# Optimization experiments

Measured on AMD Instinct MI355X. Metric: run time of the kernel, lower is better.

Reference implementation:

```python
import jax, jax.numpy as jnp
import numpy as np
import math

D_MODEL = 1024
N_HEADS = 16
SEQ = 1024
BATCH = 4


def setup_inputs() -> dict:
    key = jax.random.key(0)
    ks = jax.random.split(key, 13)
    s = 1.0 / math.sqrt(D_MODEL)  # keep logits in a sane range
    return {
        "x": jax.random.normal(ks[0], (BATCH, SEQ, D_MODEL), jnp.float32),
        "Wq": jax.random.normal(ks[1], (D_MODEL, D_MODEL), jnp.float32) * s,
        "bq": jnp.zeros((D_MODEL,), jnp.float32),
        "Wk": jax.random.normal(ks[2], (D_MODEL, D_MODEL), jnp.float32) * s,
        "bk": jnp.zeros((D_MODEL,), jnp.float32),
        "Wv": jax.random.normal(ks[3], (D_MODEL, D_MODEL), jnp.float32) * s,
        "bv": jnp.zeros((D_MODEL,), jnp.float32),
        "Wo": jax.random.normal(ks[4], (D_MODEL, D_MODEL), jnp.float32) * s,
        "bo": jnp.zeros((D_MODEL,), jnp.float32),
        "Wimp": jax.random.normal(ks[5], (N_HEADS, D_MODEL), jnp.float32) * s,
        "bimp": jnp.zeros((N_HEADS,), jnp.float32),
        "k_ema": jax.random.normal(ks[6], (SEQ, D_MODEL), jnp.float32),
        "v_ema": jax.random.normal(ks[7], (SEQ, D_MODEL), jnp.float32),
    }


def reference(x, Wq, bq, Wk, bk, Wv, bv, Wo, bo, Wimp, bimp, k_ema, v_ema):
    B, S, D = x.shape
    H = Wimp.shape[0]
    hd = D // H

    def proj(W, b):
        # [B,S,D] -> [B,H,S,hd]
        return (x @ W.T + b).reshape(B, S, H, hd).transpose(0, 2, 1, 3)

    q = proj(Wq, bq)
    k = proj(Wk, bk)
    v = proj(Wv, bv)

    scores = jnp.einsum("bhqd,bhkd->bhqk", q, k) / math.sqrt(hd)

    # importance bias: outer-sum of per-head key/value importance vectors
    k_imp = (k_ema[:S] @ Wimp.T + bimp).T  # [H, S]
    v_imp = (v_ema[:S] @ Wimp.T + bimp).T  # [H, S]
    bias = 0.5 * (k_imp[:, :, None] + v_imp[:, None, :])  # [H, S, S]
    scores = scores + 0.1 * bias[None]

    # causal mask (torch masks before bias add; -inf + finite == -inf, so equivalent)
    causal = jnp.triu(jnp.ones((S, S), bool), k=1)
    scores = jnp.where(causal, -jnp.inf, scores)

    attn = jax.nn.softmax(scores, axis=-1)
    out = jnp.einsum("bhqk,bhkd->bhqd", attn, v)
    out = out.transpose(0, 2, 1, 3).reshape(B, S, D)
    return out @ Wo.T + bo
```

## Files before the change

### kernel.cpp

```cpp
#include <hip/hip_runtime.h>
#include <hip/hip_bf16.h>
#include <math.h>

#define D_MODEL 1024
#define SEQ     1024
#define BATCH   4
#define NHEADS  16
#define HD      64

#define QSC 0.18033688f
#define BSC 0.072134752f

typedef __bf16 bf16x8 __attribute__((ext_vector_type(8)));
typedef __bf16 bf16x4 __attribute__((ext_vector_type(4)));
typedef float  f32x4  __attribute__((ext_vector_type(4)));

__device__ __forceinline__ f32x4 mfma16(bf16x8 a, bf16x8 b, f32x4 c) {
  return __builtin_amdgcn_mfma_f32_16x16x32_bf16(a, b, c, 0, 0, 0);
}

__device__ __forceinline__ void async16(__bf16* lds, const __bf16* g) {
  __builtin_amdgcn_global_load_lds(g, lds, 16, 0, 0);
}

__global__ __launch_bounds__(256) void prep_kernel(
    const float* __restrict__ x,
    const float* __restrict__ Wq, const float* __restrict__ Wk,
    const float* __restrict__ Wv, const float* __restrict__ Wo,
    const float* __restrict__ v_ema,
    const float* __restrict__ Wimp, const float* __restrict__ bimp,
    __bf16* __restrict__ x_bf, __bf16* __restrict__ wq_bf, __bf16* __restrict__ wk_bf,
    __bf16* __restrict__ wv_bf, __bf16* __restrict__ wo_bf,
    float* __restrict__ vimp) {
  const int bid = blockIdx.x;
  const int tid = threadIdx.x;
  if (bid < 4096) {
    int i = bid * 256 + tid;
    float4 v = ((const float4*)x)[i];
    bf16x4 o; o[0] = (__bf16)v.x; o[1] = (__bf16)v.y; o[2] = (__bf16)v.z; o[3] = (__bf16)v.w;
    ((bf16x4*)x_bf)[i] = o;
  } else if (bid < 8192) {
    int i = (bid - 4096) * 256 + tid;
    int sel = i >> 18;
    int j = i & 262143;
    const float* s = (sel == 0) ? Wq : (sel == 1) ? Wk : (sel == 2) ? Wv : Wo;
    __bf16* d      = (sel == 0) ? wq_bf : (sel == 1) ? wk_bf : (sel == 2) ? wv_bf : wo_bf;
    float4 v = ((const float4*)s)[j];
    bf16x4 o; o[0] = (__bf16)v.x; o[1] = (__bf16)v.y; o[2] = (__bf16)v.z; o[3] = (__bf16)v.w;
    ((bf16x4*)d)[j] = o;
  } else {
    const int s    = (bid - 8192) * 4 + (tid >> 6);
    const int lane = tid & 63;
    const float4* ve = (const float4*)(v_ema + (size_t)s * D_MODEL);
    float acc0 = 0.f, acc1 = 0.f, acc2 = 0.f, acc3 = 0.f;
    float acc4 = 0.f, acc5 = 0.f, acc6 = 0.f, acc7 = 0.f;
    float acc8 = 0.f, acc9 = 0.f, accA = 0.f, accB = 0.f;
    float accC = 0.f, accD = 0.f, accE = 0.f, accF = 0.f;
    #pragma unroll
    for (int i = 0; i < 4; i++) {
      const int c = lane + i * 64;
      float4 v = ve[c];
      #define VIMP_H(H, ACC)                                                     \
        {                                                                        \
          float4 w = ((const float4*)(Wimp + (H) * D_MODEL))[c];                 \
          ACC += v.x * w.x + v.y * w.y + v.z * w.z + v.w * w.w;                  \
        }
      VIMP_H(0, acc0)  VIMP_H(1, acc1)  VIMP_H(2, acc2)  VIMP_H(3, acc3)
      VIMP_H(4, acc4)  VIMP_H(5, acc5)  VIMP_H(6, acc6)  VIMP_H(7, acc7)
      VIMP_H(8, acc8)  VIMP_H(9, acc9)  VIMP_H(10, accA) VIMP_H(11, accB)
      VIMP_H(12, accC) VIMP_H(13, accD) VIMP_H(14, accE) VIMP_H(15, accF)
      #undef VIMP_H
    }
    #define VIMP_RED(ACC)                                                        \
      for (int mm = 32; mm >= 1; mm >>= 1) ACC += __shfl_xor(ACC, mm);
    VIMP_RED(acc0) VIMP_RED(acc1) VIMP_RED(acc2) VIMP_RED(acc3)
    VIMP_RED(acc4) VIMP_RED(acc5) VIMP_RED(acc6) VIMP_RED(acc7)
    VIMP_RED(acc8) VIMP_RED(acc9) VIMP_RED(accA) VIMP_RED(accB)
    VIMP_RED(accC) VIMP_RED(accD) VIMP_RED(accE) VIMP_RED(accF)
    #undef VIMP_RED
    if (lane == 0) {
      vimp[0  * SEQ + s] = acc0 + bimp[0];  vimp[1  * SEQ + s] = acc1 + bimp[1];
      vimp[2  * SEQ + s] = acc2 + bimp[2];  vimp[3  * SEQ + s] = acc3 + bimp[3];
      vimp[4  * SEQ + s] = acc4 + bimp[4];  vimp[5  * SEQ + s] = acc5 + bimp[5];
      vimp[6  * SEQ + s] = acc6 + bimp[6];  vimp[7  * SEQ + s] = acc7 + bimp[7];
      vimp[8  * SEQ + s] = acc8 + bimp[8];  vimp[9  * SEQ + s] = acc9 + bimp[9];
      vimp[10 * SEQ + s] = accA + bimp[10]; vimp[11 * SEQ + s] = accB + bimp[11];
      vimp[12 * SEQ + s] = accC + bimp[12]; vimp[13 * SEQ + s] = accD + bimp[13];
      vimp[14 * SEQ + s] = accE + bimp[14]; vimp[15 * SEQ + s] = accF + bimp[15];
    }
  }
}

template<bool OUT_BF16>
__global__ __launch_bounds__(256) void gemm_bt(
    const __bf16* __restrict__ A,
    const __bf16* __restrict__ W0, const __bf16* __restrict__ W1, const __bf16* __restrict__ W2,
    const float* __restrict__ b0, const float* __restrict__ b1, const float* __restrict__ b2,
    void* out0, void* out1, void* out2, float sc0, float sc1, float sc2) {
  const int z = blockIdx.z;
  const __bf16* W   = (z == 0) ? W0 : (z == 1) ? W1 : W2;
  const float* bias = (z == 0) ? b0 : (z == 1) ? b1 : b2;
  void* out         = (z == 0) ? out0 : (z == 1) ? out1 : out2;
  const float sc    = (z == 0) ? sc0 : (z == 1) ? sc1 : sc2;

  __shared__ __bf16 As[4 * 4096];
  __shared__ __bf16 Bs[4 * 4096];

  const int tid = threadIdx.x;
  const int w = tid >> 6, l = tid & 63;
  const int quad = l >> 4, l16 = l & 15;
  const int wy = w >> 1, wx = w & 1;
  const int row0 = blockIdx.y * 128;
  const int col0 = blockIdx.x * 128;

  const f32x4 fzero = {0.f, 0.f, 0.f, 0.f};
  f32x4 acc[4][4];
  for (int i = 0; i < 4; i++)
    for (int j = 0; j < 4; j++) acc[i][j] = fzero;

  const int lr = l >> 2;
  const int sw0 = (((l & 3) ^ (lr & 3)) * 8);
  const int rowA = w * 16 + lr;
  const __bf16* aptr = A + (size_t)(row0 + rowA) * D_MODEL + sw0;
  const __bf16* bptr = W + (size_t)(col0 + rowA) * D_MODEL + sw0;
  const int ldsOff = w * 512 + l * 8;

  const int rswz = (quad ^ (l16 & 3)) * 8;

  #pragma unroll
  for (int p = 0; p < 3; ++p) {
    const int off = p << 12;
    const int kk = p * 32;
    async16(&As[off + ldsOff], aptr + kk);
    async16(&As[off + 2048 + ldsOff], aptr + (size_t)64 * D_MODEL + kk);
    async16(&Bs[off + ldsOff], bptr + kk);
    async16(&Bs[off + 2048 + ldsOff], bptr + (size_t)64 * D_MODEL + kk);
  }

  #pragma unroll 4
  for (int t = 0; t < 32; ++t) {
    const int rb = (t & 3) << 12;
    if (t < 29) {
      const int sb = ((t + 3) & 3) << 12;
      const int kk = (t + 3) * 32;
      async16(&As[sb + ldsOff], aptr + kk);
      async16(&As[sb + 2048 + ldsOff], aptr + (size_t)64 * D_MODEL + kk);
      async16(&Bs[sb + ldsOff], bptr + kk);
      async16(&Bs[sb + 2048 + ldsOff], bptr + (size_t)64 * D_MODEL + kk);
      asm volatile("s_waitcnt vmcnt(12)" ::: "memory");
    } else if (t == 29) {
      asm volatile("s_waitcnt vmcnt(8)" ::: "memory");
    } else if (t == 30) {
      asm volatile("s_waitcnt vmcnt(4)" ::: "memory");
    } else {
      asm volatile("s_waitcnt vmcnt(0)" ::: "memory");
    }
    __builtin_amdgcn_s_barrier();
    bf16x8 af[4], bfr[4];
    #pragma unroll
    for (int mi = 0; mi < 4; mi++) af[mi]  = *(const bf16x8*)&As[rb + (wy * 64 + mi * 16 + l16) * 32 + rswz];
    #pragma unroll
    for (int ni = 0; ni < 4; ni++) bfr[ni] = *(const bf16x8*)&Bs[rb + (wx * 64 + ni * 16 + l16) * 32 + rswz];
    if (z == 1) {
      #pragma unroll
      for (int mi = 0; mi < 4; mi++)
        #pragma unroll
        for (int ni = 0; ni < 4; ni++)
          acc[mi][ni] = mfma16(bfr[ni], af[mi], acc[mi][ni]);
    } else {
      #pragma unroll
      for (int mi = 0; mi < 4; mi++)
        #pragma unroll
        for (int ni = 0; ni < 4; ni++)
          acc[mi][ni] = mfma16(af[mi], bfr[ni], acc[mi][ni]);
    }
    __builtin_amdgcn_s_barrier();
  }

  if (z == 1 && OUT_BF16) {
    __bf16* kp = (__bf16*)out;
    #pragma unroll
    for (int ni = 0; ni < 4; ni++) {
      const int wcolbase = col0 + wx * 64 + ni * 16 + quad * 4;
      const float4 b4 = *(const float4*)&bias[wcolbase];
      const float bb[4] = {b4.x, b4.y, b4.z, b4.w};
      #pragma unroll
      for (int mi = 0; mi < 4; mi++) {
        const int token = row0 + wy * 64 + mi * 16 + l16;
        const int bh = (token >> 10) * 16 + (wcolbase >> 6);
        const int colp = ((wcolbase & 63) + ((token & 7) << 3)) & 63;
        union { __bf16 hh[4]; uint2 uu; } pk;
        #pragma unroll
        for (int r = 0; r < 4; r++) pk.hh[r] = (__bf16)(acc[mi][ni][r] + bb[r]);
        *(uint2*)(kp + ((size_t)bh * SEQ + (token & 1023)) * HD + colp) = pk.uu;
      }
    }
  } else if (z == 2 && OUT_BF16) {
    __bf16* vp = (__bf16*)out;
    #pragma unroll
    for (int ni = 0; ni < 4; ni++) {
      const int col = col0 + wx * 64 + ni * 16 + l16;
      const float bv = bias[col];
      #pragma unroll
      for (int mi = 0; mi < 4; mi++) {
        const int token = row0 + wy * 64 + mi * 16 + quad * 4;
        const int bh = (token >> 10) * 16 + (col >> 6);
        const int chk = (token >> 6) & 15;
        const int keyp = ((token & 63) + ((col & 7) << 3)) & 63;
        const size_t base = (((size_t)bh * 16 + chk) * 64 + (col & 63)) * 64 + keyp;
        union { __bf16 hh[4]; uint2 uu; } pk;
        #pragma unroll
        for (int r = 0; r < 4; r++) pk.hh[r] = (__bf16)(acc[mi][ni][r] + bv);
        *(uint2*)(vp + base) = pk.uu;
      }
    }
  } else {
    #pragma unroll
    for (int ni = 0; ni < 4; ni++) {
      const int col = col0 + wx * 64 + ni * 16 + l16;
      const float bv = bias[col];
      #pragma unroll
      for (int mi = 0; mi < 4; mi++) {
        const int row = row0 + wy * 64 + mi * 16 + quad * 4;
        #pragma unroll
        for (int r = 0; r < 4; r++) {
          float v = (acc[mi][ni][r] + bv) * sc;
          if (OUT_BF16) ((__bf16*)out)[(size_t)(row + r) * D_MODEL + col] = (__bf16)v;
          else          ((float*)out)[(size_t)(row + r) * D_MODEL + col] = v;
        }
      }
    }
  }
}

__global__ __launch_bounds__(256, 2) void attn_kernel(
    const __bf16* __restrict__ Qb, const __bf16* __restrict__ Kp,
    const __bf16* __restrict__ Vp, const float* __restrict__ vimp,
    __bf16* __restrict__ Ob) {
  const int id = blockIdx.x;
  const int bh = id & 63;
  const int gg = id >> 6;
  const int b = bh >> 4, h = bh & 15;
  const int tid = threadIdx.x;
  const int wave = tid >> 6, lane = tid & 63;
  const int quad = lane >> 4, l16 = lane & 15;

  __shared__ __bf16 Kl[2][4096];
  __shared__ __bf16 Vl[2][4096];
  __shared__ __bf16 Ps[4][16][72];

  const __bf16* kbase = Kp + (size_t)bh * (SEQ * HD);
  const __bf16* vbase = Vp + (size_t)bh * (SEQ * HD);
  const float* vimpH = vimp + h * SEQ;

  const int rot0 = ((quad + (l16 & 7)) & 7) * 8;
  const int rot1 = ((quad + 4 + (l16 & 7)) & 7) * 8;
  const int frow = l16 * 64;

  #pragma unroll 1
  for (int grp = 0; grp < 2; grp++) {
    const int g = grp ? (15 - gg) : gg;
    const int nch = g + 1;
    const int qrow = g * 64 + wave * 16 + l16;
    const __bf16* qp = Qb + (size_t)(b * SEQ + qrow) * D_MODEL + h * HD;
    bf16x8 qa0 = *(const bf16x8*)(qp + quad * 8);
    bf16x8 qa1 = *(const bf16x8*)(qp + 32 + quad * 8);
    float l_i = 0.f;
    f32x4 o[4];
    #pragma unroll
    for (int td = 0; td < 4; td++) { o[td][0] = 0.f; o[td][1] = 0.f; o[td][2] = 0.f; o[td][3] = 0.f; }

    __syncthreads();
    async16(&Kl[0][tid * 8], kbase + tid * 8);
    async16(&Kl[0][2048 + tid * 8], kbase + 2048 + tid * 8);
    async16(&Vl[0][tid * 8], vbase + tid * 8);
    async16(&Vl[0][2048 + tid * 8], vbase + 2048 + tid * 8);

    for (int ch = 0; ch < nch; ch++) {
      const int buf = ch & 1;
      __syncthreads();
      if (ch + 1 < nch) {
        const __bf16* gk = kbase + (ch + 1) * 4096;
        const __bf16* gv = vbase + (ch + 1) * 4096;
        const int nb = buf ^ 1;
        async16(&Kl[nb][tid * 8], gk + tid * 8);
        async16(&Kl[nb][2048 + tid * 8], gk + 2048 + tid * 8);
        async16(&Vl[nb][tid * 8], gv + tid * 8);
        async16(&Vl[nb][2048 + tid * 8], gv + 2048 + tid * 8);
      }
      const int kc = ch * 64;
      float4 vi[4];
      #pragma unroll
      for (int t = 0; t < 4; t++) vi[t] = *(const float4*)(vimpH + kc + t * 16 + quad * 4);
      bf16x8 kf0[4], kf1[4];
      #pragma unroll
      for (int t = 0; t < 4; t++) {
        kf0[t] = *(const bf16x8*)&Kl[buf][t * 1024 + frow + rot0];
        kf1[t] = *(const bf16x8*)&Kl[buf][t * 1024 + frow + rot1];
      }
      bf16x8 vfr0[4], vfr1[4];
      #pragma unroll
      for (int td = 0; td < 4; td++) {
        vfr0[td] = *(const bf16x8*)&Vl[buf][td * 1024 + frow + rot0];
        vfr1[td] = *(const bf16x8*)&Vl[buf][td * 1024 + frow + rot1];
      }
      const f32x4 fz = {0.f, 0.f, 0.f, 0.f};
      float p[4][4];
      float lsum = 0.f;
      if (ch == nch - 1) {
        #pragma unroll
        for (int t = 0; t < 4; t++) {
          f32x4 sacc = fz;
          sacc = mfma16(kf0[t], qa0, sacc);
          sacc = mfma16(kf1[t], qa1, sacc);
          const float vib[4] = {vi[t].x, vi[t].y, vi[t].z, vi[t].w};
          #pragma unroll
          for (int r = 0; r < 4; r++) {
            float pp = exp2f(sacc[r] + BSC * vib[r]);
            pp = (kc + t * 16 + quad * 4 + r <= qrow) ? pp : 0.f;
            p[t][r] = pp;
            lsum += pp;
          }
        }
      } else {
        #pragma unroll
        for (int t = 0; t < 4; t++) {
          f32x4 sacc = fz;
          sacc = mfma16(kf0[t], qa0, sacc);
          sacc = mfma16(kf1[t], qa1, sacc);
          const float vib[4] = {vi[t].x, vi[t].y, vi[t].z, vi[t].w};
          #pragma unroll
          for (int r = 0; r < 4; r++) {
            float pp = exp2f(sacc[r] + BSC * vib[r]);
            p[t][r] = pp;
            lsum += pp;
          }
        }
      }
      l_i += lsum;
      #pragma unroll
      for (int t = 0; t < 4; t++) {
        union { __bf16 hh[4]; uint2 uu; } pk;
        #pragma unroll
        for (int r = 0; r < 4; r++) pk.hh[r] = (__bf16)p[t][r];
        *(uint2*)&Ps[wave][l16][t * 16 + quad * 4] = pk.uu;
      }
      bf16x8 pf0 = *(const bf16x8*)&Ps[wave][l16][quad * 8];
      bf16x8 pf1 = *(const bf16x8*)&Ps[wave][l16][32 + quad * 8];
      #pragma unroll
      for (int td = 0; td < 4; td++) {
        o[td] = mfma16(vfr0[td], pf0, o[td]);
        o[td] = mfma16(vfr1[td], pf1, o[td]);
      }
    }

    float L = l_i;
    L += __shfl_xor(L, 16);
    L += __shfl_xor(L, 32);
    const float il = 1.0f / L;
    __bf16* op = Ob + (size_t)(b * SEQ + qrow) * D_MODEL + h * HD;
    #pragma unroll
    for (int td = 0; td < 4; td++) {
      union { __bf16 hh[4]; uint2 uu; } pk;
      #pragma unroll
      for (int r = 0; r < 4; r++) pk.hh[r] = (__bf16)(o[td][r] * il);
      *(uint2*)(op + td * 16 + quad * 4) = pk.uu;
    }
  }
}

extern "C" void kernel_launch(void* const* d_in, const int* in_sizes, int n_in,
                              void* d_out, int out_size, void* d_ws, size_t ws_size,
                              hipStream_t stream) {
  const float* x     = (const float*)d_in[0];
  const float* Wq    = (const float*)d_in[1];
  const float* bq    = (const float*)d_in[2];
  const float* Wk    = (const float*)d_in[3];
  const float* bk    = (const float*)d_in[4];
  const float* Wv    = (const float*)d_in[5];
  const float* bv    = (const float*)d_in[6];
  const float* Wo    = (const float*)d_in[7];
  const float* bo    = (const float*)d_in[8];
  const float* Wimp  = (const float*)d_in[9];
  const float* bimp  = (const float*)d_in[10];
  const float* v_ema = (const float*)d_in[12];
  float* out = (float*)d_out;

  char* ws = (char*)d_ws;
  __bf16* x_bf  = (__bf16*)(ws);
  __bf16* wq_bf = (__bf16*)(ws + (8ull  << 20));
  __bf16* wk_bf = (__bf16*)(ws + (10ull << 20));
  __bf16* wv_bf = (__bf16*)(ws + (12ull << 20));
  __bf16* wo_bf = (__bf16*)(ws + (14ull << 20));
  __bf16* q_bf  = (__bf16*)(ws + (16ull << 20));
  __bf16* kp_bf = (__bf16*)(ws + (24ull << 20));
  __bf16* vp_bf = (__bf16*)(ws + (32ull << 20));
  __bf16* a_bf  = (__bf16*)(ws + (40ull << 20));
  float*  vimp  = (float*)(ws + (48ull << 20));

  prep_kernel<<<8448, 256, 0, stream>>>(
      x, Wq, Wk, Wv, Wo, v_ema, Wimp, bimp,
      x_bf, wq_bf, wk_bf, wv_bf, wo_bf, vimp);

  gemm_bt<true><<<dim3(8, 32, 3), 256, 0, stream>>>(
      x_bf, wq_bf, wk_bf, wv_bf, bq, bk, bv,
      (void*)q_bf, (void*)kp_bf, (void*)vp_bf, QSC, 1.0f, 1.0f);

  attn_kernel<<<dim3(512), 256, 0, stream>>>(
      q_bf, kp_bf, vp_bf, vimp, a_bf);

  gemm_bt<false><<<dim3(8, 32, 1), 256, 0, stream>>>(
      a_bf, wo_bf, wo_bf, wo_bf, bo, bo, bo,
      (void*)out, (void*)out, (void*)out, 1.0f, 1.0f, 1.0f);
}
```

Before: 208.7 us.

## Triple-buffer K/V pipeline across both causal query groups and vectorize GEMM epilogue stores

The attention kernel now runs the two query groups as one continuous 17-chunk stream. It uses a three-slot LDS ring for K/V tiles with prefetch distance 2 and explicit vmcnt waits in place of the per-chunk __syncthreads. The vimp bias loads are prefetched one chunk ahead, and the output is flushed when the first group finishes. The GEMM epilogue swaps MFMA operand order for the Q/output paths so each lane holds 4 consecutive columns, allowing vector bias loads and 8-byte or 16-byte stores in place of scalar strided stores. The cost is more LDS per block, which may affect occupancy, plus more complex indexing.

Result: no change. 212.8 us (+2.0%).

```diff
diff --git a/kernel.cpp b/kernel.cpp
--- a/kernel.cpp
+++ b/kernel.cpp
@@ -161,7 +161,7 @@
     for (int mi = 0; mi < 4; mi++) af[mi]  = *(const bf16x8*)&As[rb + (wy * 64 + mi * 16 + l16) * 32 + rswz];
     #pragma unroll
     for (int ni = 0; ni < 4; ni++) bfr[ni] = *(const bf16x8*)&Bs[rb + (wx * 64 + ni * 16 + l16) * 32 + rswz];
-    if (z == 1) {
+    if (z != 2) {
       #pragma unroll
       for (int mi = 0; mi < 4; mi++)
         #pragma unroll
@@ -214,20 +214,37 @@
         *(uint2*)(vp + base) = pk.uu;
       }
     }
+  } else if (OUT_BF16) {
+    __bf16* qo = (__bf16*)out;
+    #pragma unroll
+    for (int ni = 0; ni < 4; ni++) {
+      const int wcb = col0 + wx * 64 + ni * 16 + quad * 4;
+      const float4 b4 = *(const float4*)&bias[wcb];
+      const float bb[4] = {b4.x, b4.y, b4.z, b4.w};
+      #pragma unroll
+      for (int mi = 0; mi < 4; mi++) {
+        const int token = row0 + wy * 64 + mi * 16 + l16;
+        union { __bf16 hh[4]; uint2 uu; } pk;
+        #pragma unroll
+        for (int r = 0; r < 4; r++) pk.hh[r] = (__bf16)((acc[mi][ni][r] + bb[r]) * sc);
+        *(uint2*)(qo + (size_t)token * D_MODEL + wcb) = pk.uu;
+      }
+    }
   } else {
+    float* fo = (float*)out;
     #pragma unroll
     for (int ni = 0; ni < 4; ni++) {
-      const int col = col0 + wx * 64 + ni * 16 + l16;
-      const float bv = bias[col];
+      const int wcb = col0 + wx * 64 + ni * 16 + quad * 4;
+      const float4 b4 = *(const float4*)&bias[wcb];
       #pragma unroll
       for (int mi = 0; mi < 4; mi++) {
-        const int row = row0 + wy * 64 + mi * 16 + quad * 4;
-        #pragma unroll
-        for (int r = 0; r < 4; r++) {
-          float v = (acc[mi][ni][r] + bv) * sc;
-          if (OUT_BF16) ((__bf16*)out)[(size_t)(row + r) * D_MODEL + col] = (__bf16)v;
-          else          ((float*)out)[(size_t)(row + r) * D_MODEL + col] = v;
-        }
+        const int token = row0 + wy * 64 + mi * 16 + l16;
+        float4 vv;
+        vv.x = (acc[mi][ni][0] + b4.x) * sc;
+        vv.y = (acc[mi][ni][1] + b4.y) * sc;
+        vv.z = (acc[mi][ni][2] + b4.z) * sc;
+        vv.w = (acc[mi][ni][3] + b4.w) * sc;
+        *(float4*)(fo + (size_t)token * D_MODEL + wcb) = vv;
       }
     }
   }
@@ -245,8 +262,8 @@
   const int wave = tid >> 6, lane = tid & 63;
   const int quad = lane >> 4, l16 = lane & 15;
 
-  __shared__ __bf16 Kl[2][4096];
-  __shared__ __bf16 Vl[2][4096];
+  __shared__ __bf16 Kl[3][4096];
+  __shared__ __bf16 Vl[3][4096];
   __shared__ __bf16 Ps[4][16][72];
 
   const __bf16* kbase = Kp + (size_t)bh * (SEQ * HD);
@@ -257,115 +274,164 @@
   const int rot1 = ((quad + 4 + (l16 & 7)) & 7) * 8;
   const int frow = l16 * 64;
 
+  const int g0 = gg, g1 = 15 - gg;
+  const int n0 = g0 + 1;
+
+  const int qrow0 = g0 * 64 + wave * 16 + l16;
+  const int qrow1 = g1 * 64 + wave * 16 + l16;
+  const __bf16* qp0 = Qb + (size_t)(b * SEQ + qrow0) * D_MODEL + h * HD;
+  const __bf16* qp1 = Qb + (size_t)(b * SEQ + qrow1) * D_MODEL + h * HD;
+  bf16x8 qA0 = *(const bf16x8*)(qp0 + quad * 8);
+  bf16x8 qA1 = *(const bf16x8*)(qp0 + 32 + quad * 8);
+  bf16x8 qB0 = *(const bf16x8*)(qp1 + quad * 8);
+  bf16x8 qB1 = *(const bf16x8*)(qp1 + 32 + quad * 8);
+
+  async16(&Kl[0][tid * 8], kbase + tid * 8);
+  async16(&Kl[0][2048 + tid * 8], kbase + 2048 + tid * 8);
+  async16(&Vl[0][tid * 8], vbase + tid * 8);
+  async16(&Vl[0][2048 + tid * 8], vbase + 2048 + tid * 8);
+  float4 vi_c[4];
+  #pragma unroll
+  for (int t = 0; t < 4; t++) vi_c[t] = *(const float4*)(vimpH + t * 16 + quad * 4);
+  __builtin_amdgcn_sched_barrier(0);
+  {
+    const int ck1 = (1 <= g0) ? 1 : 0;
+    const __bf16* gk = kbase + (size_t)ck1 * 4096;
+    const __bf16* gv = vbase + (size_t)ck1 * 4096;
+    async16(&Kl[1][tid * 8], gk + tid * 8);
+    async16(&Kl[1][2048 + tid * 8], gk + 2048 + tid * 8);
+    async16(&Vl[1][tid * 8], gv + tid * 8);
+    async16(&Vl[1][2048 + tid * 8], gv + 2048 + tid * 8);
+  }
+
+  float l_i = 0.f;
+  f32x4 o[4];
+  #pragma unroll
+  for (int td = 0; td < 4; td++) { o[td][0] = 0.f; o[td][1] = 0.f; o[td][2] = 0.f; o[td][3] = 0.f; }
+  int qrow = qrow0;
+  bf16x8 cqa0 = qA0, cqa1 = qA1;
+
   #pragma unroll 1
-  for (int grp = 0; grp < 2; grp++) {
-    const int g = grp ? (15 - gg) : gg;
-    const int nch = g + 1;
-    const int qrow = g * 64 + wave * 16 + l16;
-    const __bf16* qp = Qb + (size_t)(b * SEQ + qrow) * D_MODEL + h * HD;
-    bf16x8 qa0 = *(const bf16x8*)(qp + quad * 8);
-    bf16x8 qa1 = *(const bf16x8*)(qp + 32 + quad * 8);
-    float l_i = 0.f;
-    f32x4 o[4];
-    #pragma unroll
-    for (int td = 0; td < 4; td++) { o[td][0] = 0.f; o[td][1] = 0.f; o[td][2] = 0.f; o[td][3] = 0.f; }
-
-    __syncthreads();
-    async16(&Kl[0][tid * 8], kbase + tid * 8);
-    async16(&Kl[0][2048 + tid * 8], kbase + 2048 + tid * 8);
-    async16(&Vl[0][tid * 8], vbase + tid * 8);
-    async16(&Vl[0][2048 + tid * 8], vbase + 2048 + tid * 8);
-
-    for (int ch = 0; ch < nch; ch++) {
-      const int buf = ch & 1;
-      __syncthreads();
-      if (ch + 1 < nch) {
-        const __bf16* gk = kbase + (ch + 1) * 4096;
-        const __bf16* gv = vbase + (ch + 1) * 4096;
-        const int nb = buf ^ 1;
-        async16(&Kl[nb][tid * 8], gk + tid * 8);
-        async16(&Kl[nb][2048 + tid * 8], gk + 2048 + tid * 8);
-        async16(&Vl[nb][tid * 8], gv + tid * 8);
-        async16(&Vl[nb][2048 + tid * 8], gv + 2048 + tid * 8);
-      }
-      const int kc = ch * 64;
-      float4 vi[4];
-      #pragma unroll
-      for (int t = 0; t < 4; t++) vi[t] = *(const float4*)(vimpH + kc + t * 16 + quad * 4);
-      bf16x8 kf0[4], kf1[4];
+  for (int c = 0; c <= 16; ++c) {
+    const int buf = c % 3;
+    if (c < 16) asm volatile("s_waitcnt vmcnt(4)" ::: "memory");
+    else        asm volatile("s_waitcnt vmcnt(0)" ::: "memory");
+    __builtin_amdgcn_s_barrier();
+    float4 vi_n[4] = {vi_c[0], vi_c[1], vi_c[2], vi_c[3]};
+    if (c + 1 <= 16) {
+      const int c1 = c + 1;
+      const int ck1 = (c1 <= g0) ? c1 : c1 - n0;
+      #pragma unroll
+      for (int t = 0; t < 4; t++)
+        vi_n[t] = *(const float4*)(vimpH + ck1 * 64 + t * 16 + quad * 4);
+    }
+    __builtin_amdgcn_sched_barrier(0);
+    if (c + 2 <= 16) {
+      const int c2 = c + 2;
+      const int ck2 = (c2 <= g0) ? c2 : c2 - n0;
+      const int nb = c2 % 3;
+      const __bf16* gk = kbase + (size_t)ck2 * 4096;
+      const __bf16* gv = vbase + (size_t)ck2 * 4096;
+      async16(&Kl[nb][tid * 8], gk + tid * 8);
+      async16(&Kl[nb][2048 + tid * 8], gk + 2048 + tid * 8);
+      async16(&Vl[nb][tid * 8], gv + tid * 8);
+      async16(&Vl[nb][2048 + tid * 8], gv + 2048 + tid * 8);
+    }
+    const int ch = (c <= g0) ? c : c - n0;
+    const int kc = ch * 64;
+    bf16x8 kf0[4], kf1[4];
+    #pragma unroll
+    for (int t = 0; t < 4; t++) {
+      kf0[t] = *(const bf16x8*)&Kl[buf][t * 1024 + frow + rot0];
+      kf1[t] = *(const bf16x8*)&Kl[buf][t * 1024 + frow + rot1];
+    }
+    bf16x8 vfr0[4], vfr1[4];
+    #pragma unroll
+    for (int td = 0; td < 4; td++) {
+      vfr0[td] = *(const bf16x8*)&Vl[buf][td * 1024 + frow + rot0];
+      vfr1[td] = *(const bf16x8*)&Vl[buf][td * 1024 + frow + rot1];
+    }
+    const f32x4 fz = {0.f, 0.f, 0.f, 0.f};
+    float p[4][4];
+    float lsum = 0.f;
+    if (c == g0 || c == 16) {
       #pragma unroll
       for (int t = 0; t < 4; t++) {
-        kf0[t] = *(const bf16x8*)&Kl[buf][t * 1024 + frow + rot0];
-        kf1[t] = *(const bf16x8*)&Kl[buf][t * 1024 + frow + rot1];
-      }
-      bf16x8 vfr0[4], vfr1[4];
+        f32x4 sacc = fz;
+        sacc = mfma16(kf0[t], cqa0, sacc);
+        sacc = mfma16(kf1[t], cqa1, sacc);
+        const float vib[4] = {vi_c[t].x, vi_c[t].y, vi_c[t].z, vi_c[t].w};
+        #pragma unroll
+        for (int r = 0; r < 4; r++) {
+          float pp = exp2f(sacc[r] + BSC * vib[r]);
+          pp = (kc + t * 16 + quad * 4 + r <= qrow) ? pp : 0.f;
+          p[t][r] = pp;
+          lsum += pp;
+        }
+      }
+    } else {
+      #pragma unroll
+      for (int t = 0; t < 4; t++) {
+        f32x4 sacc = fz;
+        sacc = mfma16(kf0[t], cqa0, sacc);
+        sacc = mfma16(kf1[t], cqa1, sacc);
+        const float vib[4] = {vi_c[t].x, vi_c[t].y, vi_c[t].z, vi_c[t].w};
+        #pragma unroll
+        for (int r = 0; r < 4; r++) {
+          float pp = exp2f(sacc[r] + BSC * vib[r]);
+          p[t][r] = pp;
+          lsum += pp;
+        }
+      }
+    }
+    l_i += lsum;
+    #pragma unroll
+    for (int t = 0; t < 4; t++) {
+      union { __bf16 hh[4]; uint2 uu; } pk;
+      #pragma unroll
+      for (int r = 0; r < 4; r++) pk.hh[r] = (__bf16)p[t][r];
+      *(uint2*)&Ps[wave][l16][t * 16 + quad * 4] = pk.uu;
+    }
+    bf16x8 pf0 = *(const bf16x8*)&Ps[wave][l16][quad * 8];
+    bf16x8 pf1 = *(const bf16x8*)&Ps[wave][l16][32 + quad * 8];
+    #pragma unroll
+    for (int td = 0; td < 4; td++) {
+      o[td] = mfma16(vfr0[td], pf0, o[td]);
+      o[td] = mfma16(vfr1[td], pf1, o[td]);
+    }
+    if (c == g0) {
+      float L = l_i;
+      L += __shfl_xor(L, 16);
+      L += __shfl_xor(L, 32);
+      const float il = 1.0f / L;
+      __bf16* op = Ob + (size_t)(b * SEQ + qrow0) * D_MODEL + h * HD;
       #pragma unroll
       for (int td = 0; td < 4; td++) {
-        vfr0[td] = *(const bf16x8*)&Vl[buf][td * 1024 + frow + rot0];
-        vfr1[td] = *(const bf16x8*)&Vl[buf][td * 1024 + frow + rot1];
-      }
-      const f32x4 fz = {0.f, 0.f, 0.f, 0.f};
-      float p[4][4];
-      float lsum = 0.f;
-      if (ch == nch - 1) {
-        #pragma unroll
-        for (int t = 0; t < 4; t++) {
-          f32x4 sacc = fz;
-          sacc = mfma16(kf0[t], qa0, sacc);
-          sacc = mfma16(kf1[t], qa1, sacc);
-          const float vib[4] = {vi[t].x, vi[t].y, vi[t].z, vi[t].w};
-          #pragma unroll
-          for (int r = 0; r < 4; r++) {
-            float pp = exp2f(sacc[r] + BSC * vib[r]);
-            pp = (kc + t * 16 + quad * 4 + r <= qrow) ? pp : 0.f;
-            p[t][r] = pp;
-            lsum += pp;
-          }
-        }
-      } else {
-        #pragma unroll
-        for (int t = 0; t < 4; t++) {
-          f32x4 sacc = fz;
-          sacc = mfma16(kf0[t], qa0, sacc);
-          sacc = mfma16(kf1[t], qa1, sacc);
-          const float vib[4] = {vi[t].x, vi[t].y, vi[t].z, vi[t].w};
-          #pragma unroll
-          for (int r = 0; r < 4; r++) {
-            float pp = exp2f(sacc[r] + BSC * vib[r]);
-            p[t][r] = pp;
-            lsum += pp;
-          }
-        }
-      }
-      l_i += lsum;
-      #pragma unroll
-      for (int t = 0; t < 4; t++) {
         union { __bf16 hh[4]; uint2 uu; } pk;
         #pragma unroll
-        for (int r = 0; r < 4; r++) pk.hh[r] = (__bf16)p[t][r];
-        *(uint2*)&Ps[wave][l16][t * 16 + quad * 4] = pk.uu;
-      }
-      bf16x8 pf0 = *(const bf16x8*)&Ps[wave][l16][quad * 8];
-      bf16x8 pf1 = *(const bf16x8*)&Ps[wave][l16][32 + quad * 8];
-      #pragma unroll
-      for (int td = 0; td < 4; td++) {
-        o[td] = mfma16(vfr0[td], pf0, o[td]);
-        o[td] = mfma16(vfr1[td], pf1, o[td]);
-      }
-    }
-
-    float L = l_i;
-    L += __shfl_xor(L, 16);
-    L += __shfl_xor(L, 32);
-    const float il = 1.0f / L;
-    __bf16* op = Ob + (size_t)(b * SEQ + qrow) * D_MODEL + h * HD;
-    #pragma unroll
-    for (int td = 0; td < 4; td++) {
-      union { __bf16 hh[4]; uint2 uu; } pk;
-      #pragma unroll
-      for (int r = 0; r < 4; r++) pk.hh[r] = (__bf16)(o[td][r] * il);
-      *(uint2*)(op + td * 16 + quad * 4) = pk.uu;
-    }
+        for (int r = 0; r < 4; r++) pk.hh[r] = (__bf16)(o[td][r] * il);
+        *(uint2*)(op + td * 16 + quad * 4) = pk.uu;
+      }
+      l_i = 0.f;
+      #pragma unroll
+      for (int td = 0; td < 4; td++) { o[td][0] = 0.f; o[td][1] = 0.f; o[td][2] = 0.f; o[td][3] = 0.f; }
+      qrow = qrow1;
+      cqa0 = qB0; cqa1 = qB1;
+    }
+    vi_c[0] = vi_n[0]; vi_c[1] = vi_n[1]; vi_c[2] = vi_n[2]; vi_c[3] = vi_n[3];
+  }
+
+  float L = l_i;
+  L += __shfl_xor(L, 16);
+  L += __shfl_xor(L, 32);
+  const float il = 1.0f / L;
+  __bf16* op = Ob + (size_t)(b * SEQ + qrow1) * D_MODEL + h * HD;
+  #pragma unroll
+  for (int td = 0; td < 4; td++) {
+    union { __bf16 hh[4]; uint2 uu; } pk;
+    #pragma unroll
+    for (int r = 0; r < 4; r++) pk.hh[r] = (__bf16)(o[td][r] * il);
+    *(uint2*)(op + td * 16 + quad * 4) = pk.uu;
   }
 }
 
```

## Share K/V chunk loads across both query groups with triple-buffered prefetch

Applied to the files above, without the earlier changes.

The attention kernel used to process its two paired query groups one after the other, reloading K/V chunks for each. It now walks the K/V chunks once and applies each chunk to both groups, so the shorter group reuses tiles already in LDS. Prefetch moves to a three-buffer, two-chunks-ahead scheme with explicit vmcnt waits and raw barriers, and exp2f is replaced by a raw v_exp_f32. The cost is more registers (two sets of accumulators and Q fragments) and more LDS, which may hurt occupancy under launch_bounds(256,2).

New measurement: 206.4 us. No clear change (-1.1%).

```diff
diff --git a/kernel.cpp b/kernel.cpp
--- a/kernel.cpp
+++ b/kernel.cpp
@@ -21,6 +21,12 @@
 
 __device__ __forceinline__ void async16(__bf16* lds, const __bf16* g) {
   __builtin_amdgcn_global_load_lds(g, lds, 16, 0, 0);
+}
+
+__device__ __forceinline__ float fexp2(float x) {
+  float r;
+  asm volatile("v_exp_f32 %0, %1" : "=v"(r) : "v"(x));
+  return r;
 }
 
 __global__ __launch_bounds__(256) void prep_kernel(
@@ -245,8 +251,8 @@
   const int wave = tid >> 6, lane = tid & 63;
   const int quad = lane >> 4, l16 = lane & 15;
 
-  __shared__ __bf16 Kl[2][4096];
-  __shared__ __bf16 Vl[2][4096];
+  __shared__ __bf16 Kl[3][4096];
+  __shared__ __bf16 Vl[3][4096];
   __shared__ __bf16 Ps[4][16][72];
 
   const __bf16* kbase = Kp + (size_t)bh * (SEQ * HD);
@@ -257,87 +263,139 @@
   const int rot1 = ((quad + 4 + (l16 & 7)) & 7) * 8;
   const int frow = l16 * 64;
 
+  const int g0 = gg, g1 = 15 - gg;
+
+  const int qrow0 = g0 * 64 + wave * 16 + l16;
+  const int qrow1 = g1 * 64 + wave * 16 + l16;
+  const __bf16* qp0 = Qb + (size_t)(b * SEQ + qrow0) * D_MODEL + h * HD;
+  const __bf16* qp1 = Qb + (size_t)(b * SEQ + qrow1) * D_MODEL + h * HD;
+  bf16x8 qA0 = *(const bf16x8*)(qp0 + quad * 8);
+  bf16x8 qA1 = *(const bf16x8*)(qp0 + 32 + quad * 8);
+  bf16x8 qB0 = *(const bf16x8*)(qp1 + quad * 8);
+  bf16x8 qB1 = *(const bf16x8*)(qp1 + 32 + quad * 8);
+
+  async16(&Kl[0][tid * 8], kbase + tid * 8);
+  async16(&Kl[0][2048 + tid * 8], kbase + 2048 + tid * 8);
+  async16(&Vl[0][tid * 8], vbase + tid * 8);
+  async16(&Vl[0][2048 + tid * 8], vbase + 2048 + tid * 8);
+  async16(&Kl[1][tid * 8], kbase + 4096 + tid * 8);
+  async16(&Kl[1][2048 + 4096 / 2 * 0 + tid * 8 + 0], kbase + 4096 + 2048 + tid * 8);
+  async16(&Vl[1][tid * 8], vbase + 4096 + tid * 8);
+  async16(&Vl[1][2048 + tid * 8], vbase + 4096 + 2048 + tid * 8);
+
+  float l0 = 0.f, l1 = 0.f;
+  f32x4 o0[4], o1[4];
+  #pragma unroll
+  for (int td = 0; td < 4; td++) {
+    o0[td][0] = 0.f; o0[td][1] = 0.f; o0[td][2] = 0.f; o0[td][3] = 0.f;
+    o1[td][0] = 0.f; o1[td][1] = 0.f; o1[td][2] = 0.f; o1[td][3] = 0.f;
+  }
+
   #pragma unroll 1
-  for (int grp = 0; grp < 2; grp++) {
-    const int g = grp ? (15 - gg) : gg;
-    const int nch = g + 1;
-    const int qrow = g * 64 + wave * 16 + l16;
-    const __bf16* qp = Qb + (size_t)(b * SEQ + qrow) * D_MODEL + h * HD;
-    bf16x8 qa0 = *(const bf16x8*)(qp + quad * 8);
-    bf16x8 qa1 = *(const bf16x8*)(qp + 32 + quad * 8);
-    float l_i = 0.f;
-    f32x4 o[4];
-    #pragma unroll
-    for (int td = 0; td < 4; td++) { o[td][0] = 0.f; o[td][1] = 0.f; o[td][2] = 0.f; o[td][3] = 0.f; }
-
-    __syncthreads();
-    async16(&Kl[0][tid * 8], kbase + tid * 8);
-    async16(&Kl[0][2048 + tid * 8], kbase + 2048 + tid * 8);
-    async16(&Vl[0][tid * 8], vbase + tid * 8);
-    async16(&Vl[0][2048 + tid * 8], vbase + 2048 + tid * 8);
-
-    for (int ch = 0; ch < nch; ch++) {
-      const int buf = ch & 1;
-      __syncthreads();
-      if (ch + 1 < nch) {
-        const __bf16* gk = kbase + (ch + 1) * 4096;
-        const __bf16* gv = vbase + (ch + 1) * 4096;
-        const int nb = buf ^ 1;
-        async16(&Kl[nb][tid * 8], gk + tid * 8);
-        async16(&Kl[nb][2048 + tid * 8], gk + 2048 + tid * 8);
-        async16(&Vl[nb][tid * 8], gv + tid * 8);
-        async16(&Vl[nb][2048 + tid * 8], gv + 2048 + tid * 8);
-      }
-      const int kc = ch * 64;
-      float4 vi[4];
-      #pragma unroll
-      for (int t = 0; t < 4; t++) vi[t] = *(const float4*)(vimpH + kc + t * 16 + quad * 4);
-      bf16x8 kf0[4], kf1[4];
-      #pragma unroll
-      for (int t = 0; t < 4; t++) {
-        kf0[t] = *(const bf16x8*)&Kl[buf][t * 1024 + frow + rot0];
-        kf1[t] = *(const bf16x8*)&Kl[buf][t * 1024 + frow + rot1];
-      }
-      bf16x8 vfr0[4], vfr1[4];
-      #pragma unroll
-      for (int td = 0; td < 4; td++) {
-        vfr0[td] = *(const bf16x8*)&Vl[buf][td * 1024 + frow + rot0];
-        vfr1[td] = *(const bf16x8*)&Vl[buf][td * 1024 + frow + rot1];
-      }
-      const f32x4 fz = {0.f, 0.f, 0.f, 0.f};
+  for (int c = 0; c <= g1; ++c) {
+    const int buf = c % 3;
+    if (c < g1) asm volatile("s_waitcnt vmcnt(4)" ::: "memory");
+    else        asm volatile("s_waitcnt vmcnt(0)" ::: "memory");
+    __builtin_amdgcn_s_barrier();
+    const int kc = c * 64;
+    float4 vi[4];
+    #pragma unroll
+    for (int t = 0; t < 4; t++) vi[t] = *(const float4*)(vimpH + kc + t * 16 + quad * 4);
+    __builtin_amdgcn_sched_barrier(0);
+    if (c + 2 <= g1) {
+      const int nb = (c + 2) % 3;
+      const __bf16* gk = kbase + (size_t)(c + 2) * 4096;
+      const __bf16* gv = vbase + (size_t)(c + 2) * 4096;
+      async16(&Kl[nb][tid * 8], gk + tid * 8);
+      async16(&Kl[nb][2048 + tid * 8], gk + 2048 + tid * 8);
+      async16(&Vl[nb][tid * 8], gv + tid * 8);
+      async16(&Vl[nb][2048 + tid * 8], gv + 2048 + tid * 8);
+    }
+    __builtin_amdgcn_sched_barrier(0);
+
+    bf16x8 kf0[4], kf1[4], vfr0[4], vfr1[4];
+    #pragma unroll
+    for (int t = 0; t < 4; t++) {
+      kf0[t] = *(const bf16x8*)&Kl[buf][t * 1024 + frow + rot0];
+      kf1[t] = *(const bf16x8*)&Kl[buf][t * 1024 + frow + rot1];
+    }
+    #pragma unroll
+    for (int td = 0; td < 4; td++) {
+      vfr0[td] = *(const bf16x8*)&Vl[buf][td * 1024 + frow + rot0];
+      vfr1[td] = *(const bf16x8*)&Vl[buf][td * 1024 + frow + rot1];
+    }
+    const f32x4 fz = {0.f, 0.f, 0.f, 0.f};
+
+    {
       float p[4][4];
       float lsum = 0.f;
-      if (ch == nch - 1) {
-        #pragma unroll
-        for (int t = 0; t < 4; t++) {
-          f32x4 sacc = fz;
-          sacc = mfma16(kf0[t], qa0, sacc);
-          sacc = mfma16(kf1[t], qa1, sacc);
-          const float vib[4] = {vi[t].x, vi[t].y, vi[t].z, vi[t].w};
+      #pragma unroll
+      for (int t = 0; t < 4; t++) {
+        f32x4 sacc = fz;
+        sacc = mfma16(kf0[t], qB0, sacc);
+        sacc = mfma16(kf1[t], qB1, sacc);
+        const float vib[4] = {vi[t].x, vi[t].y, vi[t].z, vi[t].w};
+        if (c == g1) {
           #pragma unroll
           for (int r = 0; r < 4; r++) {
-            float pp = exp2f(sacc[r] + BSC * vib[r]);
-            pp = (kc + t * 16 + quad * 4 + r <= qrow) ? pp : 0.f;
+            float pp = fexp2(sacc[r] + BSC * vib[r]);
+            pp = (kc + t * 16 + quad * 4 + r <= qrow1) ? pp : 0.f;
+            p[t][r] = pp;
+            lsum += pp;
+          }
+        } else {
+          #pragma unroll
+          for (int r = 0; r < 4; r++) {
+            float pp = fexp2(sacc[r] + BSC * vib[r]);
             p[t][r] = pp;
             lsum += pp;
           }
         }
-      } else {
-        #pragma unroll
-        for (int t = 0; t < 4; t++) {
-          f32x4 sacc = fz;
-          sacc = mfma16(kf0[t], qa0, sacc);
-          sacc = mfma16(kf1[t], qa1, sacc);
-          const float vib[4] = {vi[t].x, vi[t].y, vi[t].z, vi[t].w};
+      }
+      l1 += lsum;
+      #pragma unroll
+      for (int t = 0; t < 4; t++) {
+        union { __bf16 hh[4]; uint2 uu; } pk;
+        #pragma unroll
+        for (int r = 0; r < 4; r++) pk.hh[r] = (__bf16)p[t][r];
+        *(uint2*)&Ps[wave][l16][t * 16 + quad * 4] = pk.uu;
+      }
+      bf16x8 pf0 = *(const bf16x8*)&Ps[wave][l16][quad * 8];
+      bf16x8 pf1 = *(const bf16x8*)&Ps[wave][l16][32 + quad * 8];
+      #pragma unroll
+      for (int td = 0; td < 4; td++) {
+        o1[td] = mfma16(vfr0[td], pf0, o1[td]);
+        o1[td] = mfma16(vfr1[td], pf1, o1[td]);
+      }
+    }
+
+    if (c <= g0) {
+      float p[4][4];
+      float lsum = 0.f;
+      #pragma unroll
+      for (int t = 0; t < 4; t++) {
+        f32x4 sacc = fz;
+        sacc = mfma16(kf0[t], qA0, sacc);
+        sacc = mfma16(kf1[t], qA1, sacc);
+        const float vib[4] = {vi[t].x, vi[t].y, vi[t].z, vi[t].w};
+        if (c == g0) {
           #pragma unroll
           for (int r = 0; r < 4; r++) {
-            float pp = exp2f(sacc[r] + BSC * vib[r]);
+            float pp = fexp2(sacc[r] + BSC * vib[r]);
+            pp = (kc + t * 16 + quad * 4 + r <= qrow0) ? pp : 0.f;
+            p[t][r] = pp;
+            lsum += pp;
+          }
+        } else {
+          #pragma unroll
+          for (int r = 0; r < 4; r++) {
+            float pp = fexp2(sacc[r] + BSC * vib[r]);
             p[t][r] = pp;
             lsum += pp;
           }
         }
       }
-      l_i += lsum;
+      l0 += lsum;
       #pragma unroll
       for (int t = 0; t < 4; t++) {
         union { __bf16 hh[4]; uint2 uu; } pk;
@@ -349,23 +407,37 @@
       bf16x8 pf1 = *(const bf16x8*)&Ps[wave][l16][32 + quad * 8];
       #pragma unroll
       for (int td = 0; td < 4; td++) {
-        o[td] = mfma16(vfr0[td], pf0, o[td]);
-        o[td] = mfma16(vfr1[td], pf1, o[td]);
-      }
-    }
-
-    float L = l_i;
-    L += __shfl_xor(L, 16);
-    L += __shfl_xor(L, 32);
-    const float il = 1.0f / L;
-    __bf16* op = Ob + (size_t)(b * SEQ + qrow) * D_MODEL + h * HD;
-    #pragma unroll
-    for (int td = 0; td < 4; td++) {
-      union { __bf16 hh[4]; uint2 uu; } pk;
-      #pragma unroll
-      for (int r = 0; r < 4; r++) pk.hh[r] = (__bf16)(o[td][r] * il);
-      *(uint2*)(op + td * 16 + quad * 4) = pk.uu;
-    }
+        o0[td] = mfma16(vfr0[td], pf0, o0[td]);
+        o0[td] = mfma16(vfr1[td], pf1, o0[td]);
+      }
+      if (c == g0) {
+        float L = l0;
+        L += __shfl_xor(L, 16);
+        L += __shfl_xor(L, 32);
+        const float il = 1.0f / L;
+        __bf16* op = Ob + (size_t)(b * SEQ + qrow0) * D_MODEL + h * HD;
+        #pragma unroll
+        for (int td = 0; td < 4; td++) {
+          union { __bf16 hh[4]; uint2 uu; } pk;
+          #pragma unroll
+          for (int r = 0; r < 4; r++) pk.hh[r] = (__bf16)(o0[td][r] * il);
+          *(uint2*)(op + td * 16 + quad * 4) = pk.uu;
+        }
+      }
+    }
+  }
+
+  float L = l1;
+  L += __shfl_xor(L, 16);
+  L += __shfl_xor(L, 32);
+  const float il = 1.0f / L;
+  __bf16* op = Ob + (size_t)(b * SEQ + qrow1) * D_MODEL + h * HD;
+  #pragma unroll
+  for (int td = 0; td < 4; td++) {
+    union { __bf16 hh[4]; uint2 uu; } pk;
+    #pragma unroll
+    for (int r = 0; r < 4; r++) pk.hh[r] = (__bf16)(o1[td][r] * il);
+    *(uint2*)(op + td * 16 + quad * 4) = pk.uu;
   }
 }
 
```
